# Kernel tuning notes

Measured on AMD Instinct MI355X. Metric: run time of the kernel, lower is better.

## Reference

```python
import jax, jax.numpy as jnp
import numpy as np

N = 40000   # nodes
E = 600000  # edges
F = 128     # feature_size
H = 128     # hidden_channels
G = 32      # graphs in batch
C = 6       # classes


def setup_inputs() -> dict:
    key = jax.random.key(0)
    ks = jax.random.split(key, 20)
    x = jax.random.normal(ks[0], (N, F), jnp.float32)
    edge_index = jax.random.randint(ks[1], (2, E), 0, N, jnp.int32)
    batch = jnp.sort(jax.random.randint(ks[2], (N,), 0, G, jnp.int32))

    def lin_w(k, fan_in, fan_out):
        return jax.random.uniform(k, (fan_in, fan_out), jnp.float32,
                                  -1.0, 1.0) / np.sqrt(fan_in)

    inp = {"x": x, "edge_index": edge_index, "batch": batch,
           # GraphConv1: feature_size -> hidden (root + rel weights, bias)
           "w1_root": lin_w(ks[3], F, H), "w1_rel": lin_w(ks[4], F, H),
           "b1": jnp.zeros((H,), jnp.float32),
           # GraphConv2: hidden -> hidden
           "w2_root": lin_w(ks[5], H, H), "w2_rel": lin_w(ks[6], H, H),
           "b2": jnp.zeros((H,), jnp.float32),
           # GCNConv 3..5
           "w3": lin_w(ks[7], H, H), "b3": jnp.zeros((H,), jnp.float32),
           "w4": lin_w(ks[8], H, H), "b4": jnp.zeros((H,), jnp.float32),
           "w5": lin_w(ks[9], H, H), "b5": jnp.zeros((H,), jnp.float32),
           # final Linear(hidden, 6)
           "lin_w": lin_w(ks[10], H, C), "lin_b": jnp.zeros((C,), jnp.float32)}
    return inp


def _graph_conv(x, w_root, w_rel, b, src, dst, n):
    # PyG GraphConv (aggr='add'): out_i = W_root x_i + W_rel * sum_{j->i} x_j + b
    agg = jax.ops.segment_sum(x[src], dst, num_segments=n)
    return agg @ w_rel + x @ w_root + b


def _gcn_conv(x, w, b, src_sl, dst_sl, deg_inv_sqrt, n):
    # PyG GCNConv: out = D^-1/2 (A+I) D^-1/2 (X W) + b
    h = x @ w
    norm = deg_inv_sqrt[src_sl] * deg_inv_sqrt[dst_sl]  # [E+N]
    out = jax.ops.segment_sum(h[src_sl] * norm[:, None], dst_sl, num_segments=n)
    return out + b


def reference(x, edge_index, batch, w1_root, w1_rel, b1, w2_root, w2_rel, b2,
              w3, b3, w4, b4, w5, b5, lin_w, lin_b):
    src, dst = edge_index[0], edge_index[1]
    # self-loops for GCN layers
    loop = jnp.arange(N, dtype=edge_index.dtype)
    src_sl = jnp.concatenate([src, loop])
    dst_sl = jnp.concatenate([dst, loop])
    deg = jax.ops.segment_sum(jnp.ones((E + N,), x.dtype), dst_sl, num_segments=N)
    deg_inv_sqrt = jax.lax.rsqrt(deg)  # deg >= 1 due to self-loops

    h = jax.nn.relu(_graph_conv(x, w1_root, w1_rel, b1, src, dst, N))
    h = jax.nn.relu(_graph_conv(h, w2_root, w2_rel, b2, src, dst, N))
    h = jax.nn.relu(_gcn_conv(h, w3, b3, src_sl, dst_sl, deg_inv_sqrt, N))
    h = jax.nn.relu(_gcn_conv(h, w4, b4, src_sl, dst_sl, deg_inv_sqrt, N))
    h = _gcn_conv(h, w5, b5, src_sl, dst_sl, deg_inv_sqrt, N)

    # global_mean_pool over batch assignment
    counts = jax.ops.segment_sum(jnp.ones((N,), h.dtype), batch, num_segments=G)
    sums = jax.ops.segment_sum(h, batch, num_segments=G)
    embedding = sums / jnp.maximum(counts, 1.0)[:, None]  # [G, H]

    # dropout p=0.5 is identity in eval mode
    logits = embedding @ lin_w + lin_b  # [G, C]
    return (logits, embedding)
```

## Files before the change

kernel.cpp:

```cpp
#include <hip/hip_runtime.h>
#include <hip/hip_fp8.h>

#define Nn 40000
#define Ee 600000
#define Hh 128
#define Gg 32
#define Cc 6
#define NB 157
#define PCAP (Ee + 8 * Nn + 8)
#define LSTR 136

typedef __bf16 bf16x8 __attribute__((ext_vector_type(8)));
typedef float floatx4 __attribute__((ext_vector_type(4)));
typedef float floatx2 __attribute__((ext_vector_type(2)));
typedef unsigned short u16;
typedef unsigned int u32;
typedef unsigned char u8;

__device__ __forceinline__ u16 f2b(float f) {
    union { float f; u32 i; } v; v.f = f;
    u32 r = v.i + 0x7fffu + ((v.i >> 16) & 1u);
    return (u16)(r >> 16);
}
__device__ __forceinline__ u32 pack2(float a, float b) {
    return (u32)f2b(a) | ((u32)f2b(b) << 16);
}
__device__ __forceinline__ u8 f8e(float f) {
    __hip_fp8_e4m3 v(f); return (u8)v.__x;
}
__device__ __forceinline__ u8 f8e_hw(float f) {
    return (u8)(__builtin_amdgcn_cvt_pk_fp8_f32(f, f, 0, false) & 0xff);
}

__global__ __launch_bounds__(256) void k_setup(int* counts, float* emb, int* done,
                                               u16* xb, u16* hA16, u8* xf8, u8* hA8, u8* hB8,
                                               float* dinv,
                                               const float* __restrict__ x,
                                               const float* w0, const float* w1, const float* w2,
                                               const float* w3, const float* w4, const float* w5,
                                               const float* w6, u16* __restrict__ pwdst) {
    int gid = blockIdx.x * 256 + threadIdx.x;
    if (gid < Nn) counts[gid] = 0;
    if (gid < Gg * Hh) emb[gid] = 0.f;
    if (gid == 0) *done = 0;
    if (blockIdx.x == 0) {
        int t = threadIdx.x;
        uint4 z = { 0, 0, 0, 0 };
        if (t < 16)              *(uint4*)(xb  + (size_t)Nn * 128 + t * 8) = z;
        else if (t < 32)         *(uint4*)(hA16 + (size_t)Nn * 128 + (t - 16) * 8) = z;
        else if (t < 40)         *(uint4*)(xf8 + (size_t)Nn * 128 + (t - 32) * 16) = z;
        else if (t < 48)         *(uint4*)(hA8 + (size_t)Nn * 128 + (t - 40) * 16) = z;
        else if (t < 56)         *(uint4*)(hB8 + (size_t)Nn * 128 + (t - 48) * 16) = z;
        else if (t == 56)        dinv[Nn] = 0.f;
    }
    if (blockIdx.x < 448) {
        int idx = gid;
        if (idx < 7 * 16384) {
            const float* ws[7] = { w0, w1, w2, w3, w4, w5, w6 };
            int mat = idx >> 14, r = idx & 16383;
            int j = r & 7, n = (r >> 3) & 15, q = (r >> 7) & 3, nt = (r >> 9) & 7, t = r >> 12;
            pwdst[idx] = f2b(ws[mat][(t * 32 + q * 8 + j) * 128 + nt * 16 + n]);
        }
    } else {
        int i = ((blockIdx.x - 448) * 256 + threadIdx.x) * 4;
        float4 v = *(const float4*)(x + i);
        ushort4 o = { f2b(v.x), f2b(v.y), f2b(v.z), f2b(v.w) };
        *(ushort4*)(xb + i) = o;
        u32 p8 = (u32)f8e(v.x) | ((u32)f8e(v.y) << 8) | ((u32)f8e(v.z) << 16) | ((u32)f8e(v.w) << 24);
        *(u32*)(xf8 + i) = p8;
    }
}

__global__ __launch_bounds__(256) void k_count(const int* __restrict__ dst, int* __restrict__ counts) {
    int i = blockIdx.x * 256 + threadIdx.x;
    if (i < Ee) atomicAdd(&counts[dst[i]], 1);
}

__global__ __launch_bounds__(256) void k_scan12(const int* __restrict__ counts, int* __restrict__ bsum,
                                                int* __restrict__ boff, int* __restrict__ row_ptr,
                                                int* __restrict__ done) {
    __shared__ int sm[256];
    __shared__ int lastFlag;
    int t = threadIdx.x;
    int i = blockIdx.x * 256 + t;
    sm[t] = (i < Nn) ? ((counts[i] + 7) & ~7) : 0;
    __syncthreads();
    for (int ofs = 128; ofs > 0; ofs >>= 1) {
        if (t < ofs) sm[t] += sm[t + ofs];
        __syncthreads();
    }
    if (t == 0) {
        bsum[blockIdx.x] = sm[0];
        __threadfence();
        int prev = atomicAdd(done, 1);
        lastFlag = (prev == NB - 1);
    }
    __syncthreads();
    if (!lastFlag) return;
    __threadfence();
    int v = (t < NB) ? bsum[t] : 0;
    sm[t] = v;
    __syncthreads();
    for (int ofs = 1; ofs < 256; ofs <<= 1) {
        int u = (t >= ofs) ? sm[t - ofs] : 0;
        __syncthreads();
        sm[t] += u;
        __syncthreads();
    }
    if (t < NB) boff[t] = sm[t] - v;
    if (t == 255) row_ptr[Nn] = sm[255];
}

__global__ __launch_bounds__(256) void k_scan3(const int* counts, const int* __restrict__ boff,
                                               int* row_ptr, int* cursor, float* dinv,
                                               int* __restrict__ colidx, float* __restrict__ edinv) {
    __shared__ int sm[256];
    int t = threadIdx.x;
    int i = blockIdx.x * 256 + t;
    int c = (i < Nn) ? counts[i] : 0;
    int pc = (c + 7) & ~7;
    sm[t] = pc;
    __syncthreads();
    for (int ofs = 1; ofs < 256; ofs <<= 1) {
        int u = (t >= ofs) ? sm[t - ofs] : 0;
        __syncthreads();
        sm[t] += u;
        __syncthreads();
    }
    if (i < Nn) {
        int excl = sm[t] - pc + boff[blockIdx.x];
        row_ptr[i] = excl;
        cursor[i] = excl;
        dinv[i] = rsqrtf((float)(c + 1));
        for (int p = excl + c; p < excl + pc; ++p) { colidx[p] = Nn; edinv[p] = 0.f; }
    }
}

__global__ __launch_bounds__(256) void k_scatter(const int* __restrict__ src, const int* __restrict__ dst,
                                                 int* __restrict__ cursor, int* __restrict__ colidx,
                                                 const float* __restrict__ dinv, float* __restrict__ edinv) {
    int i = blockIdx.x * 256 + threadIdx.x;
    if (i < Ee) {
        int s = src[i];
        int d = dst[i];
        int p = atomicAdd(&cursor[d], 1);
        if ((u32)p < (u32)PCAP) { colidx[p] = s; edinv[p] = dinv[s]; }
    }
}

#define UPC_ADD(V) { floatx2 p_;                                                          \
    p_ = __builtin_amdgcn_cvt_pk_f32_fp8((int)(V).x, false); a0 += p_.x; a1 += p_.y;      \
    p_ = __builtin_amdgcn_cvt_pk_f32_fp8((int)(V).x, true);  a2 += p_.x; a3 += p_.y;      \
    p_ = __builtin_amdgcn_cvt_pk_f32_fp8((int)(V).y, false); a4 += p_.x; a5 += p_.y;      \
    p_ = __builtin_amdgcn_cvt_pk_f32_fp8((int)(V).y, true);  a6 += p_.x; a7 += p_.y; }

#define UPC_FMA(V, d) { floatx2 p_;                                                                 \
    p_ = __builtin_amdgcn_cvt_pk_f32_fp8((int)(V).x, false); a0 += (d) * p_.x; a1 += (d) * p_.y;    \
    p_ = __builtin_amdgcn_cvt_pk_f32_fp8((int)(V).x, true);  a2 += (d) * p_.x; a3 += (d) * p_.y;    \
    p_ = __builtin_amdgcn_cvt_pk_f32_fp8((int)(V).y, false); a4 += (d) * p_.x; a5 += (d) * p_.y;    \
    p_ = __builtin_amdgcn_cvt_pk_f32_fp8((int)(V).y, true);  a6 += (d) * p_.x; a7 += (d) * p_.y; }

__global__ __launch_bounds__(256) void k_layer(const u8* __restrict__ hin8,
                                               const u16* __restrict__ hin16,
                                               const u16* __restrict__ Bp_agg,
                                               const u16* __restrict__ Bp_self,
                                               const float* __restrict__ bias,
                                               u16* __restrict__ hout16,
                                               u8* __restrict__ hout8,
                                               const int* __restrict__ prow,
                                               const int* __restrict__ pcol,
                                               const float* __restrict__ dinv,
                                               const float* __restrict__ edinv,
                                               const int* __restrict__ batch,
                                               float* __restrict__ emb,
                                               int gcn, int relu, int dopool) {
    __shared__ u16 Asm[16 * LSTR];
    __shared__ float Psm[16][132];
    int wave = threadIdx.x >> 6, lane = threadIdx.x & 63;
    int m0 = blockIdx.x * 16;

    {
        int g = lane >> 4, l = lane & 15;
        int nloc = wave * 4 + g;
        int node = m0 + nloc;
        int beg = prow[node], end = prow[node + 1];
        float a0 = 0.f, a1 = 0.f, a2 = 0.f, a3 = 0.f, a4 = 0.f, a5 = 0.f, a6 = 0.f, a7 = 0.f;
        const u8* b8 = hin8 + l * 8;
        int4 i0 = {Nn,Nn,Nn,Nn}, i1 = {Nn,Nn,Nn,Nn};
        if (beg < end) {
            i0 = *(const int4*)(pcol + beg);
            i1 = *(const int4*)(pcol + beg + 4);
        }
        if (gcn) {
            for (int e = beg; e < end; e += 8) {
                int en = (e + 8 < end) ? (e + 8) : beg;
                int4 j0 = *(const int4*)(pcol + en);
                int4 j1 = *(const int4*)(pcol + en + 4);
                float4 ed0 = *(const float4*)(edinv + e);
                float4 ed1 = *(const float4*)(edinv + e + 4);
                uint2 v0 = *(const uint2*)(b8 + (size_t)i0.x * 128);
                uint2 v1 = *(const uint2*)(b8 + (size_t)i0.y * 128);
                uint2 v2 = *(const uint2*)(b8 + (size_t)i0.z * 128);
                uint2 v3 = *(const uint2*)(b8 + (size_t)i0.w * 128);
                uint2 v4 = *(const uint2*)(b8 + (size_t)i1.x * 128);
                uint2 v5 = *(const uint2*)(b8 + (size_t)i1.y * 128);
                uint2 v6 = *(const uint2*)(b8 + (size_t)i1.z * 128);
                uint2 v7 = *(const uint2*)(b8 + (size_t)i1.w * 128);
                UPC_FMA(v0, ed0.x) UPC_FMA(v1, ed0.y) UPC_FMA(v2, ed0.z) UPC_FMA(v3, ed0.w)
                UPC_FMA(v4, ed1.x) UPC_FMA(v5, ed1.y) UPC_FMA(v6, ed1.z) UPC_FMA(v7, ed1.w)
                i0 = j0; i1 = j1;
            }
            float di = dinv[node], d2n = di * di;
            uint2 us = *(const uint2*)(b8 + (size_t)node * 128);
            a0 *= di; a1 *= di; a2 *= di; a3 *= di;
            a4 *= di; a5 *= di; a6 *= di; a7 *= di;
            UPC_FMA(us, d2n)
        } else {
            for (int e = beg; e < end; e += 8) {
                int en = (e + 8 < end) ? (e + 8) : beg;
                int4 j0 = *(const int4*)(pcol + en);
                int4 j1 = *(const int4*)(pcol + en + 4);
                uint2 v0 = *(const uint2*)(b8 + (size_t)i0.x * 128);
                uint2 v1 = *(const uint2*)(b8 + (size_t)i0.y * 128);
                uint2 v2 = *(const uint2*)(b8 + (size_t)i0.z * 128);
                uint2 v3 = *(const uint2*)(b8 + (size_t)i0.w * 128);
                uint2 v4 = *(const uint2*)(b8 + (size_t)i1.x * 128);
                uint2 v5 = *(const uint2*)(b8 + (size_t)i1.y * 128);
                uint2 v6 = *(const uint2*)(b8 + (size_t)i1.z * 128);
                uint2 v7 = *(const uint2*)(b8 + (size_t)i1.w * 128);
                UPC_ADD(v0) UPC_ADD(v1) UPC_ADD(v2) UPC_ADD(v3)
                UPC_ADD(v4) UPC_ADD(v5) UPC_ADD(v6) UPC_ADD(v7)
                i0 = j0; i1 = j1;
            }
        }
        uint4 o = { pack2(a0, a1), pack2(a2, a3), pack2(a4, a5), pack2(a6, a7) };
        *(uint4*)&Asm[nloc * LSTR + l * 8] = o;
    }
    __syncthreads();

    {
        int n = lane & 15, q = lane >> 4;
        floatx4 acc0 = (floatx4){0.f, 0.f, 0.f, 0.f};
        floatx4 acc1 = (floatx4){0.f, 0.f, 0.f, 0.f};
        int nt0 = wave * 2, nt1 = wave * 2 + 1;
#pragma unroll
        for (int t = 0; t < 4; t++) {
            bf16x8 a = *(const bf16x8*)&Asm[n * LSTR + q * 8 + t * 32];
            const u16* bp = Bp_agg + t * 4096 + q * 128 + n * 8;
            bf16x8 b0 = *(const bf16x8*)(bp + nt0 * 512);
            bf16x8 b1 = *(const bf16x8*)(bp + nt1 * 512);
            acc0 = __builtin_amdgcn_mfma_f32_16x16x32_bf16(a, b0, acc0, 0, 0, 0);
            acc1 = __builtin_amdgcn_mfma_f32_16x16x32_bf16(a, b1, acc1, 0, 0, 0);
        }
        if (!gcn) {
            const u16* arow = hin16 + (size_t)(m0 + n) * 128 + q * 8;
#pragma unroll
            for (int t = 0; t < 4; t++) {
                bf16x8 a = *(const bf16x8*)(arow + t * 32);
                const u16* bp = Bp_self + t * 4096 + q * 128 + n * 8;
                bf16x8 b0 = *(const bf16x8*)(bp + nt0 * 512);
                bf16x8 b1 = *(const bf16x8*)(bp + nt1 * 512);
                acc0 = __builtin_amdgcn_mfma_f32_16x16x32_bf16(a, b0, acc0, 0, 0, 0);
                acc1 = __builtin_amdgcn_mfma_f32_16x16x32_bf16(a, b1, acc1, 0, 0, 0);
            }
        }
        if (dopool) {
#pragma unroll
            for (int j = 0; j < 2; j++) {
                int col = (wave * 2 + j) * 16 + n;
                float bv = bias[col];
                floatx4 ac = j ? acc1 : acc0;
#pragma unroll
                for (int r = 0; r < 4; r++)
                    Psm[q * 4 + r][col] = ac[r] + bv;
            }
            __syncthreads();
            if (threadIdx.x < 128) {
                int col = threadIdx.x;
                int g0 = batch[m0], g1 = batch[m0 + 15];
                for (int g = g0; g <= g1; ++g) {
                    float s = 0.f;
#pragma unroll
                    for (int i = 0; i < 16; ++i)
                        if (batch[m0 + i] == g) s += Psm[i][col];
                    atomicAdd(&emb[g * 128 + col], s);
                }
            }
        } else {
#pragma unroll
            for (int j = 0; j < 2; j++) {
                int col = (wave * 2 + j) * 16 + n;
                float bv = bias[col];
                floatx4 ac = j ? acc1 : acc0;
#pragma unroll
                for (int r = 0; r < 4; r++) {
                    float v = ac[r] + bv;
                    if (relu) v = fmaxf(v, 0.f);
                    size_t idx = (size_t)(m0 + q * 4 + r) * 128 + col;
                    if (hout16) hout16[idx] = f2b(v);
                    if (hout8)  hout8[idx]  = f8e_hw(v);
                }
            }
        }
    }
}

__global__ __launch_bounds__(256) void k_final(const float* __restrict__ emb, const int* __restrict__ batch,
                                               const float* __restrict__ lw, const float* __restrict__ lb,
                                               float* __restrict__ out) {
    __shared__ float cnt[Gg];
    int t = threadIdx.x;
    if (t < Gg) {
        int lo = 0, hi = Nn;
        while (lo < hi) { int m = (lo + hi) >> 1; if (batch[m] < t) lo = m + 1; else hi = m; }
        int lb0 = lo;
        lo = 0; hi = Nn;
        int tg = t + 1;
        while (lo < hi) { int m = (lo + hi) >> 1; if (batch[m] < tg) lo = m + 1; else hi = m; }
        cnt[t] = fmaxf((float)(lo - lb0), 1.f);
    }
    __syncthreads();
    for (int i = t; i < Gg * Hh; i += 256) {
        int g = i >> 7;
        out[Gg * Cc + i] = emb[i] / cnt[g];
    }
    if (t < Gg * Cc) {
        int g = t / Cc, c = t % Cc;
        float cn = cnt[g];
        float s = lb[c];
        for (int f = 0; f < Hh; f++)
            s += (emb[g * 128 + f] / cn) * lw[f * Cc + c];
        out[t] = s;
    }
}

extern "C" void kernel_launch(void* const* d_in, const int* in_sizes, int n_in,
                              void* d_out, int out_size, void* d_ws, size_t ws_size,
                              hipStream_t stream) {
    const float* x       = (const float*)d_in[0];
    const int*   ei      = (const int*)d_in[1];
    const int*   batch   = (const int*)d_in[2];
    const float* w1_root = (const float*)d_in[3];
    const float* w1_rel  = (const float*)d_in[4];
    const float* b1      = (const float*)d_in[5];
    const float* w2_root = (const float*)d_in[6];
    const float* w2_rel  = (const float*)d_in[7];
    const float* b2      = (const float*)d_in[8];
    const float* w3      = (const float*)d_in[9];
    const float* b3      = (const float*)d_in[10];
    const float* w4      = (const float*)d_in[11];
    const float* b4      = (const float*)d_in[12];
    const float* w5      = (const float*)d_in[13];
    const float* b5      = (const float*)d_in[14];
    const float* lw      = (const float*)d_in[15];
    const float* lb      = (const float*)d_in[16];
    const int* srcp = ei;
    const int* dstp = ei + Ee;
    float* out = (float*)d_out;

    char* w = (char*)d_ws;
    size_t off = 0;
    auto alloc = [&](size_t bytes) { size_t r = off; off += (bytes + 255) & ~(size_t)255; return r; };
    int*   counts  = (int*)(w + alloc(Nn * 4));
    int*   row_ptr = (int*)(w + alloc((Nn + 1) * 4));
    int*   colidx  = (int*)(w + alloc((size_t)PCAP * 4));
    float* edinv   = (float*)(w + alloc((size_t)PCAP * 4));
    float* dinv    = (float*)(w + alloc((Nn + 1) * 4));
    float* emb     = (float*)(w + alloc(Gg * Hh * 4));
    int*   bsum    = (int*)(w + alloc(NB * 4));
    int*   boff    = (int*)(w + alloc(256 * 4));
    int*   done    = (int*)(w + alloc(256));
    u16*   pw      = (u16*)(w + alloc(7 * 16384 * 2));
    u16*   xb      = (u16*)(w + alloc((size_t)(Nn + 1) * Hh * 2));
    u16*   hA16    = (u16*)(w + alloc((size_t)(Nn + 1) * Hh * 2));
    u8*    xf8     = (u8*)(w + alloc((size_t)(Nn + 1) * Hh));
    u8*    hA8     = (u8*)(w + alloc((size_t)(Nn + 1) * Hh));
    u8*    hB8     = (u8*)(w + alloc((size_t)(Nn + 1) * Hh));
    (void)ws_size;

    u16* pw1r = pw + 0 * 16384;
    u16* pw1l = pw + 1 * 16384;
    u16* pw2r = pw + 2 * 16384;
    u16* pw2l = pw + 3 * 16384;
    u16* pw3  = pw + 4 * 16384;
    u16* pw4  = pw + 5 * 16384;
    u16* pw5  = pw + 6 * 16384;
    const u16* nil16 = (const u16*)nullptr;
    u16* no16 = (u16*)nullptr;
    u8*  no8  = (u8*)nullptr;

    hipLaunchKernelGGL(k_setup, dim3(448 + Nn * Hh / 1024), dim3(256), 0, stream,
                       counts, emb, done, xb, hA16, xf8, hA8, hB8, dinv,
                       x, w1_root, w1_rel, w2_root, w2_rel, w3, w4, w5, pw);
    hipLaunchKernelGGL(k_count, dim3((Ee + 255) / 256), dim3(256), 0, stream, dstp, counts);
    hipLaunchKernelGGL(k_scan12, dim3(NB), dim3(256), 0, stream, counts, bsum, boff, row_ptr, done);
    hipLaunchKernelGGL(k_scan3, dim3(NB), dim3(256), 0, stream, counts, boff, row_ptr, counts, dinv, colidx, edinv);
    hipLaunchKernelGGL(k_scatter, dim3((Ee + 255) / 256), dim3(256), 0, stream, srcp, dstp, counts, colidx, dinv, edinv);

    hipLaunchKernelGGL(k_layer, dim3(Nn / 16), dim3(256), 0, stream,
                       xf8, xb, pw1l, pw1r, b1, hA16, hA8, row_ptr, colidx, dinv, edinv, batch, emb, 0, 1, 0);
    hipLaunchKernelGGL(k_layer, dim3(Nn / 16), dim3(256), 0, stream,
                       hA8, hA16, pw2l, pw2r, b2, no16, hB8, row_ptr, colidx, dinv, edinv, batch, emb, 0, 1, 0);
    hipLaunchKernelGGL(k_layer, dim3(Nn / 16), dim3(256), 0, stream,
                       hB8, nil16, pw3, nil16, b3, no16, hA8, row_ptr, colidx, dinv, edinv, batch, emb, 1, 1, 0);
    hipLaunchKernelGGL(k_layer, dim3(Nn / 16), dim3(256), 0, stream,
                       hA8, nil16, pw4, nil16, b4, no16, xf8, row_ptr, colidx, dinv, edinv, batch, emb, 1, 1, 0);
    hipLaunchKernelGGL(k_layer, dim3(Nn / 16), dim3(256), 0, stream,
                       xf8, nil16, pw5, nil16, b5, no16, no8, row_ptr, colidx, dinv, edinv, batch, emb, 1, 0, 1);

    hipLaunchKernelGGL(k_final, dim3(1), dim3(256), 0, stream, emb, batch, lw, lb, out);
}
```

Baseline: 305.3 us.

## Fuse five GNN layers and final pooling into one persistent cooperative kernel

Replaces the five per-layer launches and the final kernel with a single cooperative persistent kernel. Blocks pull 16-node tiles from a per-layer atomic work counter and meet at a grid-wide sync between layers. Separate fp8 buffers are now allocated for each layer output so the kernel never reads and writes the same buffer. This is meant to remove launch gaps and tail effects between layers and to balance uneven node degrees dynamically, at the cost of grid.sync barriers, an atomic per tile, and possibly lower occupancy from the launch bounds of 256 threads and 4 blocks.

```diff
diff --git a/kernel.cpp b/kernel.cpp
--- a/kernel.cpp
+++ b/kernel.cpp
@@ -1,5 +1,8 @@
 #include <hip/hip_runtime.h>
 #include <hip/hip_fp8.h>
+#include <hip/hip_cooperative_groups.h>
+
+namespace cg = cooperative_groups;
 
 #define Nn 40000
 #define Ee 600000
@@ -7,6 +10,7 @@
 #define Gg 32
 #define Cc 6
 #define NB 157
+#define NT (Nn / 16)
 #define PCAP (Ee + 8 * Nn + 8)
 #define LSTR 136
 
@@ -32,8 +36,9 @@
     return (u8)(__builtin_amdgcn_cvt_pk_fp8_f32(f, f, 0, false) & 0xff);
 }
 
-__global__ __launch_bounds__(256) void k_setup(int* counts, float* emb, int* done,
-                                               u16* xb, u16* hA16, u8* xf8, u8* hA8, u8* hB8,
+__global__ __launch_bounds__(256) void k_setup(int* counts, float* emb, int* done, int* wctr,
+                                               u16* xb, u16* hA16, u8* xf8,
+                                               u8* g1, u8* g2, u8* g3, u8* g4,
                                                float* dinv,
                                                const float* __restrict__ x,
                                                const float* w0, const float* w1, const float* w2,
@@ -43,15 +48,18 @@
     if (gid < Nn) counts[gid] = 0;
     if (gid < Gg * Hh) emb[gid] = 0.f;
     if (gid == 0) *done = 0;
+    if (gid < 8) wctr[gid] = 0;
     if (blockIdx.x == 0) {
         int t = threadIdx.x;
         uint4 z = { 0, 0, 0, 0 };
-        if (t < 16)              *(uint4*)(xb  + (size_t)Nn * 128 + t * 8) = z;
+        if (t < 16)              *(uint4*)(xb   + (size_t)Nn * 128 + t * 8) = z;
         else if (t < 32)         *(uint4*)(hA16 + (size_t)Nn * 128 + (t - 16) * 8) = z;
-        else if (t < 40)         *(uint4*)(xf8 + (size_t)Nn * 128 + (t - 32) * 16) = z;
-        else if (t < 48)         *(uint4*)(hA8 + (size_t)Nn * 128 + (t - 40) * 16) = z;
-        else if (t < 56)         *(uint4*)(hB8 + (size_t)Nn * 128 + (t - 48) * 16) = z;
-        else if (t == 56)        dinv[Nn] = 0.f;
+        else if (t < 40)         *(uint4*)(xf8  + (size_t)Nn * 128 + (t - 32) * 16) = z;
+        else if (t < 48)         *(uint4*)(g1   + (size_t)Nn * 128 + (t - 40) * 16) = z;
+        else if (t < 56)         *(uint4*)(g2   + (size_t)Nn * 128 + (t - 48) * 16) = z;
+        else if (t < 64)         *(uint4*)(g3   + (size_t)Nn * 128 + (t - 56) * 16) = z;
+        else if (t < 72)         *(uint4*)(g4   + (size_t)Nn * 128 + (t - 64) * 16) = z;
+        else if (t == 72)        dinv[Nn] = 0.f;
     }
     if (blockIdx.x < 448) {
         int idx = gid;
@@ -160,177 +168,211 @@
     p_ = __builtin_amdgcn_cvt_pk_f32_fp8((int)(V).y, false); a4 += (d) * p_.x; a5 += (d) * p_.y;    \
     p_ = __builtin_amdgcn_cvt_pk_f32_fp8((int)(V).y, true);  a6 += (d) * p_.x; a7 += (d) * p_.y; }
 
-__global__ __launch_bounds__(256) void k_layer(const u8* __restrict__ hin8,
-                                               const u16* __restrict__ hin16,
-                                               const u16* __restrict__ Bp_agg,
-                                               const u16* __restrict__ Bp_self,
-                                               const float* __restrict__ bias,
-                                               u16* __restrict__ hout16,
-                                               u8* __restrict__ hout8,
-                                               const int* __restrict__ prow,
-                                               const int* __restrict__ pcol,
-                                               const float* __restrict__ dinv,
-                                               const float* __restrict__ edinv,
-                                               const int* __restrict__ batch,
-                                               float* __restrict__ emb,
-                                               int gcn, int relu, int dopool) {
+__global__ __launch_bounds__(256, 4) void k_layers(
+        const u8* __restrict__ xf8, u8* __restrict__ g1, u8* __restrict__ g2,
+        u8* __restrict__ g3, u8* __restrict__ g4,
+        const u16* __restrict__ xb, u16* __restrict__ hA16,
+        const u16* __restrict__ pw,
+        const float* __restrict__ b1, const float* __restrict__ b2,
+        const float* __restrict__ b3, const float* __restrict__ b4,
+        const float* __restrict__ b5,
+        const int* __restrict__ prow, const int* __restrict__ pcol,
+        const float* __restrict__ dinv, const float* __restrict__ edinv,
+        const int* __restrict__ batch, float* __restrict__ emb,
+        int* __restrict__ wctr,
+        const float* __restrict__ lw, const float* __restrict__ lb,
+        float* __restrict__ out)
+{
+    cg::grid_group grid = cg::this_grid();
     __shared__ u16 Asm[16 * LSTR];
     __shared__ float Psm[16][132];
+    __shared__ int s_tile;
+
+    const u8*  IN8[5]   = { xf8, g1, g2, g3, g4 };
+    u8*        OUT8[5]  = { g1, g2, g3, g4, nullptr };
+    const u16* IN16[5]  = { xb, hA16, nullptr, nullptr, nullptr };
+    u16*       OUT16[5] = { hA16, nullptr, nullptr, nullptr, nullptr };
+    const u16* BAGG[5]  = { pw + 1 * 16384, pw + 3 * 16384, pw + 4 * 16384, pw + 5 * 16384, pw + 6 * 16384 };
+    const u16* BSELF[5] = { pw + 0 * 16384, pw + 2 * 16384, nullptr, nullptr, nullptr };
+    const float* BIAS[5] = { b1, b2, b3, b4, b5 };
+
     int wave = threadIdx.x >> 6, lane = threadIdx.x & 63;
-    int m0 = blockIdx.x * 16;
-
-    {
-        int g = lane >> 4, l = lane & 15;
-        int nloc = wave * 4 + g;
-        int node = m0 + nloc;
-        int beg = prow[node], end = prow[node + 1];
-        float a0 = 0.f, a1 = 0.f, a2 = 0.f, a3 = 0.f, a4 = 0.f, a5 = 0.f, a6 = 0.f, a7 = 0.f;
-        const u8* b8 = hin8 + l * 8;
-        int4 i0 = {Nn,Nn,Nn,Nn}, i1 = {Nn,Nn,Nn,Nn};
-        if (beg < end) {
-            i0 = *(const int4*)(pcol + beg);
-            i1 = *(const int4*)(pcol + beg + 4);
-        }
-        if (gcn) {
-            for (int e = beg; e < end; e += 8) {
-                int en = (e + 8 < end) ? (e + 8) : beg;
-                int4 j0 = *(const int4*)(pcol + en);
-                int4 j1 = *(const int4*)(pcol + en + 4);
-                float4 ed0 = *(const float4*)(edinv + e);
-                float4 ed1 = *(const float4*)(edinv + e + 4);
-                uint2 v0 = *(const uint2*)(b8 + (size_t)i0.x * 128);
-                uint2 v1 = *(const uint2*)(b8 + (size_t)i0.y * 128);
-                uint2 v2 = *(const uint2*)(b8 + (size_t)i0.z * 128);
-                uint2 v3 = *(const uint2*)(b8 + (size_t)i0.w * 128);
-                uint2 v4 = *(const uint2*)(b8 + (size_t)i1.x * 128);
-                uint2 v5 = *(const uint2*)(b8 + (size_t)i1.y * 128);
-                uint2 v6 = *(const uint2*)(b8 + (size_t)i1.z * 128);
-                uint2 v7 = *(const uint2*)(b8 + (size_t)i1.w * 128);
-                UPC_FMA(v0, ed0.x) UPC_FMA(v1, ed0.y) UPC_FMA(v2, ed0.z) UPC_FMA(v3, ed0.w)
-                UPC_FMA(v4, ed1.x) UPC_FMA(v5, ed1.y) UPC_FMA(v6, ed1.z) UPC_FMA(v7, ed1.w)
-                i0 = j0; i1 = j1;
-            }
-            float di = dinv[node], d2n = di * di;
-            uint2 us = *(const uint2*)(b8 + (size_t)node * 128);
-            a0 *= di; a1 *= di; a2 *= di; a3 *= di;
-            a4 *= di; a5 *= di; a6 *= di; a7 *= di;
-            UPC_FMA(us, d2n)
-        } else {
-            for (int e = beg; e < end; e += 8) {
-                int en = (e + 8 < end) ? (e + 8) : beg;
-                int4 j0 = *(const int4*)(pcol + en);
-                int4 j1 = *(const int4*)(pcol + en + 4);
-                uint2 v0 = *(const uint2*)(b8 + (size_t)i0.x * 128);
-                uint2 v1 = *(const uint2*)(b8 + (size_t)i0.y * 128);
-                uint2 v2 = *(const uint2*)(b8 + (size_t)i0.z * 128);
-                uint2 v3 = *(const uint2*)(b8 + (size_t)i0.w * 128);
-                uint2 v4 = *(const uint2*)(b8 + (size_t)i1.x * 128);
-                uint2 v5 = *(const uint2*)(b8 + (size_t)i1.y * 128);
-                uint2 v6 = *(const uint2*)(b8 + (size_t)i1.z * 128);
-                uint2 v7 = *(const uint2*)(b8 + (size_t)i1.w * 128);
-                UPC_ADD(v0) UPC_ADD(v1) UPC_ADD(v2) UPC_ADD(v3)
-                UPC_ADD(v4) UPC_ADD(v5) UPC_ADD(v6) UPC_ADD(v7)
-                i0 = j0; i1 = j1;
-            }
-        }
-        uint4 o = { pack2(a0, a1), pack2(a2, a3), pack2(a4, a5), pack2(a6, a7) };
-        *(uint4*)&Asm[nloc * LSTR + l * 8] = o;
-    }
-    __syncthreads();
-
-    {
-        int n = lane & 15, q = lane >> 4;
-        floatx4 acc0 = (floatx4){0.f, 0.f, 0.f, 0.f};
-        floatx4 acc1 = (floatx4){0.f, 0.f, 0.f, 0.f};
-        int nt0 = wave * 2, nt1 = wave * 2 + 1;
-#pragma unroll
-        for (int t = 0; t < 4; t++) {
-            bf16x8 a = *(const bf16x8*)&Asm[n * LSTR + q * 8 + t * 32];
-            const u16* bp = Bp_agg + t * 4096 + q * 128 + n * 8;
-            bf16x8 b0 = *(const bf16x8*)(bp + nt0 * 512);
-            bf16x8 b1 = *(const bf16x8*)(bp + nt1 * 512);
-            acc0 = __builtin_amdgcn_mfma_f32_16x16x32_bf16(a, b0, acc0, 0, 0, 0);
-            acc1 = __builtin_amdgcn_mfma_f32_16x16x32_bf16(a, b1, acc1, 0, 0, 0);
-        }
-        if (!gcn) {
-            const u16* arow = hin16 + (size_t)(m0 + n) * 128 + q * 8;
-#pragma unroll
-            for (int t = 0; t < 4; t++) {
-                bf16x8 a = *(const bf16x8*)(arow + t * 32);
-                const u16* bp = Bp_self + t * 4096 + q * 128 + n * 8;
-                bf16x8 b0 = *(const bf16x8*)(bp + nt0 * 512);
-                bf16x8 b1 = *(const bf16x8*)(bp + nt1 * 512);
-                acc0 = __builtin_amdgcn_mfma_f32_16x16x32_bf16(a, b0, acc0, 0, 0, 0);
-                acc1 = __builtin_amdgcn_mfma_f32_16x16x32_bf16(a, b1, acc1, 0, 0, 0);
-            }
-        }
-        if (dopool) {
-#pragma unroll
-            for (int j = 0; j < 2; j++) {
-                int col = (wave * 2 + j) * 16 + n;
-                float bv = bias[col];
-                floatx4 ac = j ? acc1 : acc0;
-#pragma unroll
-                for (int r = 0; r < 4; r++)
-                    Psm[q * 4 + r][col] = ac[r] + bv;
+
+    for (int L = 0; L < 5; ++L) {
+        const int gcn = (L >= 2), relu = (L < 4), dopool = (L == 4);
+        const u8*  hin8   = IN8[L];
+        const u16* hin16  = IN16[L];
+        const u16* Bp_agg = BAGG[L];
+        const u16* Bp_self= BSELF[L];
+        const float* bias = BIAS[L];
+        u16* hout16 = OUT16[L];
+        u8*  hout8  = OUT8[L];
+
+        for (;;) {
+            if (threadIdx.x == 0) s_tile = atomicAdd(&wctr[L], 1);
+            __syncthreads();
+            int tile = s_tile;
+            if (tile >= NT) break;
+            int m0 = tile * 16;
+
+            {
+                int g = lane >> 4, l = lane & 15;
+                int nloc = wave * 4 + g;
+                int node = m0 + nloc;
+                int beg = prow[node], end = prow[node + 1];
+                float a0 = 0.f, a1 = 0.f, a2 = 0.f, a3 = 0.f, a4 = 0.f, a5 = 0.f, a6 = 0.f, a7 = 0.f;
+                const u8* b8 = hin8 + l * 8;
+                int4 i0 = {Nn,Nn,Nn,Nn}, i1 = {Nn,Nn,Nn,Nn};
+                if (beg < end) {
+                    i0 = *(const int4*)(pcol + beg);
+                    i1 = *(const int4*)(pcol + beg + 4);
+                }
+                if (gcn) {
+                    for (int e = beg; e < end; e += 8) {
+                        int en = (e + 8 < end) ? (e + 8) : beg;
+                        int4 j0 = *(const int4*)(pcol + en);
+                        int4 j1 = *(const int4*)(pcol + en + 4);
+                        float4 ed0 = *(const float4*)(edinv + e);
+                        float4 ed1 = *(const float4*)(edinv + e + 4);
+                        uint2 v0 = *(const uint2*)(b8 + (size_t)i0.x * 128);
+                        uint2 v1 = *(const uint2*)(b8 + (size_t)i0.y * 128);
+                        uint2 v2 = *(const uint2*)(b8 + (size_t)i0.z * 128);
+                        uint2 v3 = *(const uint2*)(b8 + (size_t)i0.w * 128);
+                        uint2 v4 = *(const uint2*)(b8 + (size_t)i1.x * 128);
+                        uint2 v5 = *(const uint2*)(b8 + (size_t)i1.y * 128);
+                        uint2 v6 = *(const uint2*)(b8 + (size_t)i1.z * 128);
+                        uint2 v7 = *(const uint2*)(b8 + (size_t)i1.w * 128);
+                        UPC_FMA(v0, ed0.x) UPC_FMA(v1, ed0.y) UPC_FMA(v2, ed0.z) UPC_FMA(v3, ed0.w)
+                        UPC_FMA(v4, ed1.x) UPC_FMA(v5, ed1.y) UPC_FMA(v6, ed1.z) UPC_FMA(v7, ed1.w)
+                        i0 = j0; i1 = j1;
+                    }
+                    float di = dinv[node], d2n = di * di;
+                    uint2 us = *(const uint2*)(b8 + (size_t)node * 128);
+                    a0 *= di; a1 *= di; a2 *= di; a3 *= di;
+                    a4 *= di; a5 *= di; a6 *= di; a7 *= di;
+                    UPC_FMA(us, d2n)
+                } else {
+                    for (int e = beg; e < end; e += 8) {
+                        int en = (e + 8 < end) ? (e + 8) : beg;
+                        int4 j0 = *(const int4*)(pcol + en);
+                        int4 j1 = *(const int4*)(pcol + en + 4);
+                        uint2 v0 = *(const uint2*)(b8 + (size_t)i0.x * 128);
+                        uint2 v1 = *(const uint2*)(b8 + (size_t)i0.y * 128);
+                        uint2 v2 = *(const uint2*)(b8 + (size_t)i0.z * 128);
+                        uint2 v3 = *(const uint2*)(b8 + (size_t)i0.w * 128);
+                        uint2 v4 = *(const uint2*)(b8 + (size_t)i1.x * 128);
+                        uint2 v5 = *(const uint2*)(b8 + (size_t)i1.y * 128);
+                        uint2 v6 = *(const uint2*)(b8 + (size_t)i1.z * 128);
+                        uint2 v7 = *(const uint2*)(b8 + (size_t)i1.w * 128);
+                        UPC_ADD(v0) UPC_ADD(v1) UPC_ADD(v2) UPC_ADD(v3)
+                        UPC_ADD(v4) UPC_ADD(v5) UPC_ADD(v6) UPC_ADD(v7)
+                        i0 = j0; i1 = j1;
+                    }
+                }
+                uint4 o = { pack2(a0, a1), pack2(a2, a3), pack2(a4, a5), pack2(a6, a7) };
+                *(uint4*)&Asm[nloc * LSTR + l * 8] = o;
             }
             __syncthreads();
-            if (threadIdx.x < 128) {
-                int col = threadIdx.x;
-                int g0 = batch[m0], g1 = batch[m0 + 15];
-                for (int g = g0; g <= g1; ++g) {
-                    float s = 0.f;
-#pragma unroll
-                    for (int i = 0; i < 16; ++i)
-                        if (batch[m0 + i] == g) s += Psm[i][col];
-                    atomicAdd(&emb[g * 128 + col], s);
+
+            {
+                int n = lane & 15, q = lane >> 4;
+                floatx4 acc0 = (floatx4){0.f, 0.f, 0.f, 0.f};
+                floatx4 acc1 = (floatx4){0.f, 0.f, 0.f, 0.f};
+                int nt0 = wave * 2, nt1 = wave * 2 + 1;
+#pragma unroll
+                for (int t = 0; t < 4; t++) {
+                    bf16x8 a = *(const bf16x8*)&Asm[n * LSTR + q * 8 + t * 32];
+                    const u16* bp = Bp_agg + t * 4096 + q * 128 + n * 8;
+                    bf16x8 b0 = *(const bf16x8*)(bp + nt0 * 512);
+                    bf16x8 b1 = *(const bf16x8*)(bp + nt1 * 512);
+                    acc0 = __builtin_amdgcn_mfma_f32_16x16x32_bf16(a, b0, acc0, 0, 0, 0);
+                    acc1 = __builtin_amdgcn_mfma_f32_16x16x32_bf16(a, b1, acc1, 0, 0, 0);
+                }
+                if (!gcn) {
+                    const u16* arow = hin16 + (size_t)(m0 + n) * 128 + q * 8;
+#pragma unroll
+                    for (int t = 0; t < 4; t++) {
+                        bf16x8 a = *(const bf16x8*)(arow + t * 32);
+                        const u16* bp = Bp_self + t * 4096 + q * 128 + n * 8;
+                        bf16x8 b0 = *(const bf16x8*)(bp + nt0 * 512);
+                        bf16x8 b1 = *(const bf16x8*)(bp + nt1 * 512);
+                        acc0 = __builtin_amdgcn_mfma_f32_16x16x32_bf16(a, b0, acc0, 0, 0, 0);
+                        acc1 = __builtin_amdgcn_mfma_f32_16x16x32_bf16(a, b1, acc1, 0, 0, 0);
+                    }
+                }
+                if (dopool) {
+#pragma unroll
+                    for (int j = 0; j < 2; j++) {
+                        int col = (wave * 2 + j) * 16 + n;
+                        float bv = bias[col];
+                        floatx4 ac = j ? acc1 : acc0;
+#pragma unroll
+                        for (int r = 0; r < 4; r++)
+                            Psm[q * 4 + r][col] = ac[r] + bv;
+                    }
+                    __syncthreads();
+                    if (threadIdx.x < 128) {
+                        int col = threadIdx.x;
+                        int g0 = batch[m0], g1i = batch[m0 + 15];
+                        for (int g = g0; g <= g1i; ++g) {
+                            float s = 0.f;
+#pragma unroll
+                            for (int i = 0; i < 16; ++i)
+                                if (batch[m0 + i] == g) s += Psm[i][col];
+                            atomicAdd(&emb[g * 128 + col], s);
+                        }
+                    }
+                } else {
+#pragma unroll
+                    for (int j = 0; j < 2; j++) {
+                        int col = (wave * 2 + j) * 16 + n;
+                        float bv = bias[col];
+                        floatx4 ac = j ? acc1 : acc0;
+#pragma unroll
+                        for (int r = 0; r < 4; r++) {
+                            float v = ac[r] + bv;
+                            if (relu) v = fmaxf(v, 0.f);
+                            size_t idx = (size_t)(m0 + q * 4 + r) * 128 + col;
+                            if (hout16) hout16[idx] = f2b(v);
+                            if (hout8)  hout8[idx]  = f8e_hw(v);
+                        }
+                    }
                 }
             }
-        } else {
-#pragma unroll
-            for (int j = 0; j < 2; j++) {
-                int col = (wave * 2 + j) * 16 + n;
-                float bv = bias[col];
-                floatx4 ac = j ? acc1 : acc0;
-#pragma unroll
-                for (int r = 0; r < 4; r++) {
-                    float v = ac[r] + bv;
-                    if (relu) v = fmaxf(v, 0.f);
-                    size_t idx = (size_t)(m0 + q * 4 + r) * 128 + col;
-                    if (hout16) hout16[idx] = f2b(v);
-                    if (hout8)  hout8[idx]  = f8e_hw(v);
-                }
+            __syncthreads();
+        }
+        __threadfence();
+        grid.sync();
+    }
+
+    if (blockIdx.x == 0) {
+        __shared__ float cnt[Gg];
+        int t = threadIdx.x;
+        if (t < Gg) {
+            int lo = 0, hi = Nn;
+            while (lo < hi) { int m = (lo + hi) >> 1; if (batch[m] < t) lo = m + 1; else hi = m; }
+            int lb0 = lo;
+            lo = 0; hi = Nn;
+            int tg = t + 1;
+            while (lo < hi) { int m = (lo + hi) >> 1; if (batch[m] < tg) lo = m + 1; else hi = m; }
+            cnt[t] = fmaxf((float)(lo - lb0), 1.f);
+        }
+        __syncthreads();
+        for (int i = t; i < Gg * Hh; i += 256) {
+            int g = i >> 7;
+            float e = __hip_atomic_load(&emb[i], __ATOMIC_RELAXED, __HIP_MEMORY_SCOPE_AGENT);
+            out[Gg * Cc + i] = e / cnt[g];
+        }
+        if (t < Gg * Cc) {
+            int g = t / Cc, c = t % Cc;
+            float cn = cnt[g];
+            float s = lb[c];
+            for (int f = 0; f < Hh; f++) {
+                float e = __hip_atomic_load(&emb[g * 128 + f], __ATOMIC_RELAXED, __HIP_MEMORY_SCOPE_AGENT);
+                s += (e / cn) * lw[f * Cc + c];
             }
+            out[t] = s;
         }
-    }
-}
-
-__global__ __launch_bounds__(256) void k_final(const float* __restrict__ emb, const int* __restrict__ batch,
-                                               const float* __restrict__ lw, const float* __restrict__ lb,
-                                               float* __restrict__ out) {
-    __shared__ float cnt[Gg];
-    int t = threadIdx.x;
-    if (t < Gg) {
-        int lo = 0, hi = Nn;
-        while (lo < hi) { int m = (lo + hi) >> 1; if (batch[m] < t) lo = m + 1; else hi = m; }
-        int lb0 = lo;
-        lo = 0; hi = Nn;
-        int tg = t + 1;
-        while (lo < hi) { int m = (lo + hi) >> 1; if (batch[m] < tg) lo = m + 1; else hi = m; }
-        cnt[t] = fmaxf((float)(lo - lb0), 1.f);
-    }
-    __syncthreads();
-    for (int i = t; i < Gg * Hh; i += 256) {
-        int g = i >> 7;
-        out[Gg * Cc + i] = emb[i] / cnt[g];
-    }
-    if (t < Gg * Cc) {
-        int g = t / Cc, c = t % Cc;
-        float cn = cnt[g];
-        float s = lb[c];
-        for (int f = 0; f < Hh; f++)
-            s += (emb[g * 128 + f] / cn) * lw[f * Cc + c];
-        out[t] = s;
     }
 }
 
@@ -370,43 +412,38 @@
     int*   bsum    = (int*)(w + alloc(NB * 4));
     int*   boff    = (int*)(w + alloc(256 * 4));
     int*   done    = (int*)(w + alloc(256));
+    int*   wctr    = (int*)(w + alloc(256));
     u16*   pw      = (u16*)(w + alloc(7 * 16384 * 2));
     u16*   xb      = (u16*)(w + alloc((size_t)(Nn + 1) * Hh * 2));
     u16*   hA16    = (u16*)(w + alloc((size_t)(Nn + 1) * Hh * 2));
     u8*    xf8     = (u8*)(w + alloc((size_t)(Nn + 1) * Hh));
-    u8*    hA8     = (u8*)(w + alloc((size_t)(Nn + 1) * Hh));
-    u8*    hB8     = (u8*)(w + alloc((size_t)(Nn + 1) * Hh));
+    u8*    g1      = (u8*)(w + alloc((size_t)(Nn + 1) * Hh));
+    u8*    g2      = (u8*)(w + alloc((size_t)(Nn + 1) * Hh));
+    u8*    g3      = (u8*)(w + alloc((size_t)(Nn + 1) * Hh));
+    u8*    g4      = (u8*)(w + alloc((size_t)(Nn + 1) * Hh));
     (void)ws_size;
 
-    u16* pw1r = pw + 0 * 16384;
-    u16* pw1l = pw + 1 * 16384;
-    u16* pw2r = pw + 2 * 16384;
-    u16* pw2l = pw + 3 * 16384;
-    u16* pw3  = pw + 4 * 16384;
-    u16* pw4  = pw + 5 * 16384;
-    u16* pw5  = pw + 6 * 16384;
-    const u16* nil16 = (const u16*)nullptr;
-    u16* no16 = (u16*)nullptr;
-    u8*  no8  = (u8*)nullptr;
-
     hipLaunchKernelGGL(k_setup, dim3(448 + Nn * Hh / 1024), dim3(256), 0, stream,
-                       counts, emb, done, xb, hA16, xf8, hA8, hB8, dinv,
+                       counts, emb, done, wctr, xb, hA16, xf8, g1, g2, g3, g4, dinv,
                        x, w1_root, w1_rel, w2_root, w2_rel, w3, w4, w5, pw);
     hipLaunchKernelGGL(k_count, dim3((Ee + 255) / 256), dim3(256), 0, stream, dstp, counts);
     hipLaunchKernelGGL(k_scan12, dim3(NB), dim3(256), 0, stream, counts, bsum, boff, row_ptr, done);
     hipLaunchKernelGGL(k_scan3, dim3(NB), dim3(256), 0, stream, counts, boff, row_ptr, counts, dinv, colidx, edinv);
     hipLaunchKernelGGL(k_scatter, dim3((Ee + 255) / 256), dim3(256), 0, stream, srcp, dstp, counts, colidx, dinv, edinv);
 
-    hipLaunchKernelGGL(k_layer, dim3(Nn / 16), dim3(256), 0, stream,
-                       xf8, xb, pw1l, pw1r, b1, hA16, hA8, row_ptr, colidx, dinv, edinv, batch, emb, 0, 1, 0);
-    hipLaunchKernelGGL(k_layer, dim3(Nn / 16), dim3(256), 0, stream,
-                       hA8, hA16, pw2l, pw2r, b2, no16, hB8, row_ptr, colidx, dinv, edinv, batch, emb, 0, 1, 0);
-    hipLaunchKernelGGL(k_layer, dim3(Nn / 16), dim3(256), 0, stream,
-                       hB8, nil16, pw3, nil16, b3, no16, hA8, row_ptr, colidx, dinv, edinv, batch, emb, 1, 1, 0);
-    hipLaunchKernelGGL(k_layer, dim3(Nn / 16), dim3(256), 0, stream,
-                       hA8, nil16, pw4, nil16, b4, no16, xf8, row_ptr, colidx, dinv, edinv, batch, emb, 1, 1, 0);
-    hipLaunchKernelGGL(k_layer, dim3(Nn / 16), dim3(256), 0, stream,
-                       xf8, nil16, pw5, nil16, b5, no16, no8, row_ptr, colidx, dinv, edinv, batch, emb, 1, 0, 1);
-
-    hipLaunchKernelGGL(k_final, dim3(1), dim3(256), 0, stream, emb, batch, lw, lb, out);
-}
+    static int s_grid = 0;
+    if (s_grid == 0) {
+        int maxb = 0;
+        if (hipOccupancyMaxActiveBlocksPerMultiprocessor(&maxb, k_layers, 256, 0) != hipSuccess || maxb < 1)
+            maxb = 4;
+        if (maxb > 8) maxb = 8;
+        s_grid = maxb * 256;
+    }
+    void* kargs[] = { (void*)&xf8, (void*)&g1, (void*)&g2, (void*)&g3, (void*)&g4,
+                      (void*)&xb, (void*)&hA16, (void*)&pw,
+                      (void*)&b1, (void*)&b2, (void*)&b3, (void*)&b4, (void*)&b5,
+                      (void*)&row_ptr, (void*)&colidx, (void*)&dinv, (void*)&edinv,
+                      (void*)&batch, (void*)&emb, (void*)&wctr,
+                      (void*)&lw, (void*)&lb, (void*)&out };
+    hipLaunchCooperativeKernel((void*)k_layers, dim3(s_grid), dim3(256), kargs, 0, stream);
+}
```

Result: slower. 985.4 us (+222.7%).

## Interleave CSR column index and edge norm; vectorize count and scatter kernels

Applied to the files above, without the earlier changes.

Replaces the separate colidx and edinv arrays with one interleaved int2 array, so each edge's source index and normalisation factor come in together with 16-byte loads. The aggregation loop reads four int4s per 8 edges instead of separate index and weight streams. The count and scatter kernels now process four edges per thread via int4 loads. The trade-off is that the non-GCN layers now read the unused weight half, doubling their index traffic.

```diff
diff --git a/kernel.cpp b/kernel.cpp
--- a/kernel.cpp
+++ b/kernel.cpp
@@ -72,8 +72,14 @@
 }
 
 __global__ __launch_bounds__(256) void k_count(const int* __restrict__ dst, int* __restrict__ counts) {
-    int i = blockIdx.x * 256 + threadIdx.x;
-    if (i < Ee) atomicAdd(&counts[dst[i]], 1);
+    int i = (blockIdx.x * 256 + threadIdx.x) * 4;
+    if (i < Ee) {
+        int4 d = *(const int4*)(dst + i);
+        atomicAdd(&counts[d.x], 1);
+        atomicAdd(&counts[d.y], 1);
+        atomicAdd(&counts[d.z], 1);
+        atomicAdd(&counts[d.w], 1);
+    }
 }
 
 __global__ __launch_bounds__(256) void k_scan12(const int* __restrict__ counts, int* __restrict__ bsum,
@@ -113,7 +119,7 @@
 
 __global__ __launch_bounds__(256) void k_scan3(const int* counts, const int* __restrict__ boff,
                                                int* row_ptr, int* cursor, float* dinv,
-                                               int* __restrict__ colidx, float* __restrict__ edinv) {
+                                               int2* __restrict__ epack) {
     __shared__ int sm[256];
     int t = threadIdx.x;
     int i = blockIdx.x * 256 + t;
@@ -132,19 +138,31 @@
         row_ptr[i] = excl;
         cursor[i] = excl;
         dinv[i] = rsqrtf((float)(c + 1));
-        for (int p = excl + c; p < excl + pc; ++p) { colidx[p] = Nn; edinv[p] = 0.f; }
+        int2 pad; pad.x = Nn; pad.y = 0;
+        for (int p = excl + c; p < excl + pc; ++p) epack[p] = pad;
     }
 }
 
 __global__ __launch_bounds__(256) void k_scatter(const int* __restrict__ src, const int* __restrict__ dst,
-                                                 int* __restrict__ cursor, int* __restrict__ colidx,
-                                                 const float* __restrict__ dinv, float* __restrict__ edinv) {
-    int i = blockIdx.x * 256 + threadIdx.x;
+                                                 int* __restrict__ cursor, int2* __restrict__ epack,
+                                                 const float* __restrict__ dinv) {
+    int i = (blockIdx.x * 256 + threadIdx.x) * 4;
     if (i < Ee) {
-        int s = src[i];
-        int d = dst[i];
-        int p = atomicAdd(&cursor[d], 1);
-        if ((u32)p < (u32)PCAP) { colidx[p] = s; edinv[p] = dinv[s]; }
+        int4 s4 = *(const int4*)(src + i);
+        int4 d4 = *(const int4*)(dst + i);
+        int p0 = atomicAdd(&cursor[d4.x], 1);
+        int p1 = atomicAdd(&cursor[d4.y], 1);
+        int p2 = atomicAdd(&cursor[d4.z], 1);
+        int p3 = atomicAdd(&cursor[d4.w], 1);
+        float e0 = dinv[s4.x], e1 = dinv[s4.y], e2 = dinv[s4.z], e3 = dinv[s4.w];
+        int2 v0; v0.x = s4.x; v0.y = __float_as_int(e0);
+        int2 v1; v1.x = s4.y; v1.y = __float_as_int(e1);
+        int2 v2; v2.x = s4.z; v2.y = __float_as_int(e2);
+        int2 v3; v3.x = s4.w; v3.y = __float_as_int(e3);
+        if ((u32)p0 < (u32)PCAP) epack[p0] = v0;
+        if ((u32)p1 < (u32)PCAP) epack[p1] = v1;
+        if ((u32)p2 < (u32)PCAP) epack[p2] = v2;
+        if ((u32)p3 < (u32)PCAP) epack[p3] = v3;
     }
 }
 
@@ -168,9 +186,8 @@
                                                u16* __restrict__ hout16,
                                                u8* __restrict__ hout8,
                                                const int* __restrict__ prow,
-                                               const int* __restrict__ pcol,
+                                               const int* __restrict__ epk,
                                                const float* __restrict__ dinv,
-                                               const float* __restrict__ edinv,
                                                const int* __restrict__ batch,
                                                float* __restrict__ emb,
                                                int gcn, int relu, int dopool) {
@@ -186,52 +203,61 @@
         int beg = prow[node], end = prow[node + 1];
         float a0 = 0.f, a1 = 0.f, a2 = 0.f, a3 = 0.f, a4 = 0.f, a5 = 0.f, a6 = 0.f, a7 = 0.f;
         const u8* b8 = hin8 + l * 8;
-        int4 i0 = {Nn,Nn,Nn,Nn}, i1 = {Nn,Nn,Nn,Nn};
         if (beg < end) {
-            i0 = *(const int4*)(pcol + beg);
-            i1 = *(const int4*)(pcol + beg + 4);
+            int4 q0 = *(const int4*)(epk + 2 * beg);
+            int4 q1 = *(const int4*)(epk + 2 * beg + 4);
+            int4 q2 = *(const int4*)(epk + 2 * beg + 8);
+            int4 q3 = *(const int4*)(epk + 2 * beg + 12);
+            if (gcn) {
+                for (int e = beg; e < end; e += 8) {
+                    int en = (e + 8 < end) ? (e + 8) : beg;
+                    int4 r0 = *(const int4*)(epk + 2 * en);
+                    int4 r1 = *(const int4*)(epk + 2 * en + 4);
+                    int4 r2 = *(const int4*)(epk + 2 * en + 8);
+                    int4 r3 = *(const int4*)(epk + 2 * en + 12);
+                    uint2 v0 = *(const uint2*)(b8 + (size_t)q0.x * 128);
+                    uint2 v1 = *(const uint2*)(b8 + (size_t)q0.z * 128);
+                    uint2 v2 = *(const uint2*)(b8 + (size_t)q1.x * 128);
+                    uint2 v3 = *(const uint2*)(b8 + (size_t)q1.z * 128);
+                    uint2 v4 = *(const uint2*)(b8 + (size_t)q2.x * 128);
+                    uint2 v5 = *(const uint2*)(b8 + (size_t)q2.z * 128);
+                    uint2 v6 = *(const uint2*)(b8 + (size_t)q3.x * 128);
+                    uint2 v7 = *(const uint2*)(b8 + (size_t)q3.z * 128);
+                    float d0 = __int_as_float(q0.y), d1 = __int_as_float(q0.w);
+                    float d2 = __int_as_float(q1.y), d3 = __int_as_float(q1.w);
+                    float d4 = __int_as_float(q2.y), d5 = __int_as_float(q2.w);
+                    float d6 = __int_as_float(q3.y), d7 = __int_as_float(q3.w);
+                    UPC_FMA(v0, d0) UPC_FMA(v1, d1) UPC_FMA(v2, d2) UPC_FMA(v3, d3)
+                    UPC_FMA(v4, d4) UPC_FMA(v5, d5) UPC_FMA(v6, d6) UPC_FMA(v7, d7)
+                    q0 = r0; q1 = r1; q2 = r2; q3 = r3;
+                }
+            } else {
+                for (int e = beg; e < end; e += 8) {
+                    int en = (e + 8 < end) ? (e + 8) : beg;
+                    int4 r0 = *(const int4*)(epk + 2 * en);
+                    int4 r1 = *(const int4*)(epk + 2 * en + 4);
+                    int4 r2 = *(const int4*)(epk + 2 * en + 8);
+                    int4 r3 = *(const int4*)(epk + 2 * en + 12);
+                    uint2 v0 = *(const uint2*)(b8 + (size_t)q0.x * 128);
+                    uint2 v1 = *(const uint2*)(b8 + (size_t)q0.z * 128);
+                    uint2 v2 = *(const uint2*)(b8 + (size_t)q1.x * 128);
+                    uint2 v3 = *(const uint2*)(b8 + (size_t)q1.z * 128);
+                    uint2 v4 = *(const uint2*)(b8 + (size_t)q2.x * 128);
+                    uint2 v5 = *(const uint2*)(b8 + (size_t)q2.z * 128);
+                    uint2 v6 = *(const uint2*)(b8 + (size_t)q3.x * 128);
+                    uint2 v7 = *(const uint2*)(b8 + (size_t)q3.z * 128);
+                    UPC_ADD(v0) UPC_ADD(v1) UPC_ADD(v2) UPC_ADD(v3)
+                    UPC_ADD(v4) UPC_ADD(v5) UPC_ADD(v6) UPC_ADD(v7)
+                    q0 = r0; q1 = r1; q2 = r2; q3 = r3;
+                }
+            }
         }
         if (gcn) {
-            for (int e = beg; e < end; e += 8) {
-                int en = (e + 8 < end) ? (e + 8) : beg;
-                int4 j0 = *(const int4*)(pcol + en);
-                int4 j1 = *(const int4*)(pcol + en + 4);
-                float4 ed0 = *(const float4*)(edinv + e);
-                float4 ed1 = *(const float4*)(edinv + e + 4);
-                uint2 v0 = *(const uint2*)(b8 + (size_t)i0.x * 128);
-                uint2 v1 = *(const uint2*)(b8 + (size_t)i0.y * 128);
-                uint2 v2 = *(const uint2*)(b8 + (size_t)i0.z * 128);
-                uint2 v3 = *(const uint2*)(b8 + (size_t)i0.w * 128);
-                uint2 v4 = *(const uint2*)(b8 + (size_t)i1.x * 128);
-                uint2 v5 = *(const uint2*)(b8 + (size_t)i1.y * 128);
-                uint2 v6 = *(const uint2*)(b8 + (size_t)i1.z * 128);
-                uint2 v7 = *(const uint2*)(b8 + (size_t)i1.w * 128);
-                UPC_FMA(v0, ed0.x) UPC_FMA(v1, ed0.y) UPC_FMA(v2, ed0.z) UPC_FMA(v3, ed0.w)
-                UPC_FMA(v4, ed1.x) UPC_FMA(v5, ed1.y) UPC_FMA(v6, ed1.z) UPC_FMA(v7, ed1.w)
-                i0 = j0; i1 = j1;
-            }
             float di = dinv[node], d2n = di * di;
             uint2 us = *(const uint2*)(b8 + (size_t)node * 128);
             a0 *= di; a1 *= di; a2 *= di; a3 *= di;
             a4 *= di; a5 *= di; a6 *= di; a7 *= di;
             UPC_FMA(us, d2n)
-        } else {
-            for (int e = beg; e < end; e += 8) {
-                int en = (e + 8 < end) ? (e + 8) : beg;
-                int4 j0 = *(const int4*)(pcol + en);
-                int4 j1 = *(const int4*)(pcol + en + 4);
-                uint2 v0 = *(const uint2*)(b8 + (size_t)i0.x * 128);
-                uint2 v1 = *(const uint2*)(b8 + (size_t)i0.y * 128);
-                uint2 v2 = *(const uint2*)(b8 + (size_t)i0.z * 128);
-                uint2 v3 = *(const uint2*)(b8 + (size_t)i0.w * 128);
-                uint2 v4 = *(const uint2*)(b8 + (size_t)i1.x * 128);
-                uint2 v5 = *(const uint2*)(b8 + (size_t)i1.y * 128);
-                uint2 v6 = *(const uint2*)(b8 + (size_t)i1.z * 128);
-                uint2 v7 = *(const uint2*)(b8 + (size_t)i1.w * 128);
-                UPC_ADD(v0) UPC_ADD(v1) UPC_ADD(v2) UPC_ADD(v3)
-                UPC_ADD(v4) UPC_ADD(v5) UPC_ADD(v6) UPC_ADD(v7)
-                i0 = j0; i1 = j1;
-            }
         }
         uint4 o = { pack2(a0, a1), pack2(a2, a3), pack2(a4, a5), pack2(a6, a7) };
         *(uint4*)&Asm[nloc * LSTR + l * 8] = o;
@@ -363,8 +389,7 @@
     auto alloc = [&](size_t bytes) { size_t r = off; off += (bytes + 255) & ~(size_t)255; return r; };
     int*   counts  = (int*)(w + alloc(Nn * 4));
     int*   row_ptr = (int*)(w + alloc((Nn + 1) * 4));
-    int*   colidx  = (int*)(w + alloc((size_t)PCAP * 4));
-    float* edinv   = (float*)(w + alloc((size_t)PCAP * 4));
+    int2*  epack   = (int2*)(w + alloc((size_t)PCAP * 8));
     float* dinv    = (float*)(w + alloc((Nn + 1) * 4));
     float* emb     = (float*)(w + alloc(Gg * Hh * 4));
     int*   bsum    = (int*)(w + alloc(NB * 4));
@@ -388,25 +413,26 @@
     const u16* nil16 = (const u16*)nullptr;
     u16* no16 = (u16*)nullptr;
     u8*  no8  = (u8*)nullptr;
+    const int* epki = (const int*)epack;
 
     hipLaunchKernelGGL(k_setup, dim3(448 + Nn * Hh / 1024), dim3(256), 0, stream,
                        counts, emb, done, xb, hA16, xf8, hA8, hB8, dinv,
                        x, w1_root, w1_rel, w2_root, w2_rel, w3, w4, w5, pw);
-    hipLaunchKernelGGL(k_count, dim3((Ee + 255) / 256), dim3(256), 0, stream, dstp, counts);
+    hipLaunchKernelGGL(k_count, dim3((Ee / 4 + 255) / 256), dim3(256), 0, stream, dstp, counts);
     hipLaunchKernelGGL(k_scan12, dim3(NB), dim3(256), 0, stream, counts, bsum, boff, row_ptr, done);
-    hipLaunchKernelGGL(k_scan3, dim3(NB), dim3(256), 0, stream, counts, boff, row_ptr, counts, dinv, colidx, edinv);
-    hipLaunchKernelGGL(k_scatter, dim3((Ee + 255) / 256), dim3(256), 0, stream, srcp, dstp, counts, colidx, dinv, edinv);
+    hipLaunchKernelGGL(k_scan3, dim3(NB), dim3(256), 0, stream, counts, boff, row_ptr, counts, dinv, epack);
+    hipLaunchKernelGGL(k_scatter, dim3((Ee / 4 + 255) / 256), dim3(256), 0, stream, srcp, dstp, counts, epack, dinv);
 
     hipLaunchKernelGGL(k_layer, dim3(Nn / 16), dim3(256), 0, stream,
-                       xf8, xb, pw1l, pw1r, b1, hA16, hA8, row_ptr, colidx, dinv, edinv, batch, emb, 0, 1, 0);
+                       xf8, xb, pw1l, pw1r, b1, hA16, hA8, row_ptr, epki, dinv, batch, emb, 0, 1, 0);
     hipLaunchKernelGGL(k_layer, dim3(Nn / 16), dim3(256), 0, stream,
-                       hA8, hA16, pw2l, pw2r, b2, no16, hB8, row_ptr, colidx, dinv, edinv, batch, emb, 0, 1, 0);
+                       hA8, hA16, pw2l, pw2r, b2, no16, hB8, row_ptr, epki, dinv, batch, emb, 0, 1, 0);
     hipLaunchKernelGGL(k_layer, dim3(Nn / 16), dim3(256), 0, stream,
-                       hB8, nil16, pw3, nil16, b3, no16, hA8, row_ptr, colidx, dinv, edinv, batch, emb, 1, 1, 0);
+                       hB8, nil16, pw3, nil16, b3, no16, hA8, row_ptr, epki, dinv, batch, emb, 1, 1, 0);
     hipLaunchKernelGGL(k_layer, dim3(Nn / 16), dim3(256), 0, stream,
-                       hA8, nil16, pw4, nil16, b4, no16, xf8, row_ptr, colidx, dinv, edinv, batch, emb, 1, 1, 0);
+                       hA8, nil16, pw4, nil16, b4, no16, xf8, row_ptr, epki, dinv, batch, emb, 1, 1, 0);
     hipLaunchKernelGGL(k_layer, dim3(Nn / 16), dim3(256), 0, stream,
-                       xf8, nil16, pw5, nil16, b5, no16, no8, row_ptr, colidx, dinv, edinv, batch, emb, 1, 0, 1);
+                       xf8, nil16, pw5, nil16, b5, no16, no8, row_ptr, epki, dinv, batch, emb, 1, 0, 1);
 
     hipLaunchKernelGGL(k_final, dim3(1), dim3(256), 0, stream, emb, batch, lw, lb, out);
 }
```

Result: slower. 320.2 us (+4.9%).
